# Optimization experiments

Measured on AMD Instinct MI355X. Metric: run time of the kernel, lower is better.

Reference implementation:

```python
import jax, jax.numpy as jnp
import numpy as np

N_REC = 12288  # 12 * nside^2, nside=32


def _mlp(x, w1, b1, w2, b2):
    # two-layer MLP with SiLU, as in GraphCast-style edge embedders
    return jnp.dot(jax.nn.silu(jnp.dot(x, w1) + b1), w2) + b2


def setup_inputs() -> dict:
    key = jax.random.key(0)
    ks = jax.random.split(key, 12)
    B, E, D_X, D_EDGE = 2, 393216, 128, 4
    EDGE_IN, EDGE_OUT, LIN_OUT = D_EDGE + D_X, 256, 256

    def glorot(k, shape):
        fan = shape[0] + shape[1]
        return jax.random.normal(k, shape, jnp.float32) * jnp.sqrt(2.0 / fan)

    return {
        "x": jax.random.normal(ks[0], (B, E, D_X), jnp.float32),
        "edge_attr": jax.random.normal(ks[1], (E, D_EDGE), jnp.float32),
        "edge_index": jax.random.randint(ks[2], (2, E), 0, N_REC, jnp.int64),
        "w1e": glorot(ks[3], (EDGE_IN, EDGE_OUT)),
        "b1e": jnp.zeros((EDGE_OUT,), jnp.float32),
        "w2e": glorot(ks[4], (EDGE_OUT, EDGE_OUT)),
        "b2e": jnp.zeros((EDGE_OUT,), jnp.float32),
        "w1f": glorot(ks[5], (EDGE_OUT, LIN_OUT)),
        "b1f": jnp.zeros((LIN_OUT,), jnp.float32),
        "w2f": glorot(ks[6], (LIN_OUT, LIN_OUT)),
        "b2f": jnp.zeros((LIN_OUT,), jnp.float32),
    }


def reference(x, edge_attr, edge_index, w1e, b1e, w2e, b2e, w1f, b1f, w2f, b2f):
    B = x.shape[0]
    # broadcast edge_attr over batch and concat with per-edge grid features
    ea = jnp.broadcast_to(edge_attr[None], (B,) + edge_attr.shape)  # [B,E,d_edge]
    v_g_prime = jnp.concatenate([ea, x], axis=-1)                    # [B,E,edge_in]
    v_g = _mlp(v_g_prime, w1e, b1e, w2e, b2e)                        # [B,E,edge_out]
    # scatter-sum edges into receiver nodes (edge_index[1]) along dim 1
    recv = edge_index[1]
    v_m_sum = jnp.zeros((B, N_REC, v_g.shape[-1]), v_g.dtype).at[:, recv].add(v_g)
    return _mlp(v_m_sum, w1f, b1f, w2f, b2f)                         # [B,N_REC,lin_out]
```

## Files before the change

### kernel.cpp

```cpp
#include <hip/hip_runtime.h>
#include <hip/hip_bf16.h>

#define E_EDGES 393216
#define NRECV   12288
#define DX      128
#define BATCH   2

typedef short bf16x8 __attribute__((ext_vector_type(8)));
typedef float f32x4  __attribute__((ext_vector_type(4)));

__device__ __forceinline__ unsigned short f2bf(float f) {
  union { float f; unsigned u; } v; v.f = f;
  unsigned r = v.u + 0x7FFFu + ((v.u >> 16) & 1u);
  return (unsigned short)(r >> 16);
}

__device__ __forceinline__ unsigned pk2(float a, float b) {
  __hip_bfloat162 h = __float22bfloat162_rn(make_float2(a, b));
  union { __hip_bfloat162 h; unsigned u; } c; c.h = h;
  return c.u;
}

__device__ __forceinline__ float silu_f(float v) {
  float e = __builtin_amdgcn_exp2f(v * -1.44269504089f);
  return v * __builtin_amdgcn_rcpf(1.0f + e);
}

__global__ __launch_bounds__(256) void zero_kernel(float4* __restrict__ p, int n4) {
  int i = blockIdx.x * 256 + threadIdx.x;
  int stride = gridDim.x * 256;
  float4 z = make_float4(0.f, 0.f, 0.f, 0.f);
  for (; i < n4; i += stride) p[i] = z;
}

__global__ __launch_bounds__(256) void prep_kernel(
    const float* __restrict__ w1e, const float* __restrict__ b1e,
    const float* __restrict__ w2e, const float* __restrict__ w1f,
    const float* __restrict__ w2f,
    unsigned short* __restrict__ w1sw, unsigned short* __restrict__ w2esw,
    unsigned short* __restrict__ w1fsw, unsigned short* __restrict__ w2fsw,
    const int* __restrict__ recv, int* __restrict__ cnt) {
  int blk = blockIdx.x;
  if (blk < 160) {
    int t = blk * 256 + threadIdx.x;
    int j = t & 7, l = (t >> 3) & 63, rest = t >> 9;
    int nf = rest & 15, ks = rest >> 4;
    int k = ks * 32 + (l >> 4) * 8 + j;
    int n = nf * 16 + (l & 15);
    float v = (k < 132) ? w1e[k * 256 + n] : (k == 132 ? b1e[n] : 0.0f);
    w1sw[t] = f2bf(v);
  } else if (blk < 928) {
    int g = blk - 160;
    int which = g >> 8;
    int t = (g & 255) * 256 + threadIdx.x;
    const float* W = (which == 0) ? w2e : (which == 1) ? w1f : w2f;
    unsigned short* O = (which == 0) ? w2esw : (which == 1) ? w1fsw : w2fsw;
    int j = t & 7, l = (t >> 3) & 63, rest = t >> 9;
    int nf = rest & 15, ks = rest >> 4;
    int k = ks * 32 + (l >> 4) * 8 + j;
    int n = nf * 16 + (l & 15);
    O[t] = f2bf(W[k * 256 + n]);
  } else {
    int e = (blk - 928) * 256 + threadIdx.x;
    if (e < E_EDGES) atomicAdd(&cnt[recv[e]], 1);
  }
}

__global__ __launch_bounds__(256) void scan_kernel(const int* __restrict__ cnt,
                                                   int* __restrict__ head) {
  __shared__ int ts[256];
  const int t = threadIdx.x;
  const int base = t * 48;
  int s = 0;
#pragma unroll
  for (int i = 0; i < 48; ++i) s += cnt[base + i];
  ts[t] = s;
  __syncthreads();
  for (int d = 1; d < 256; d <<= 1) {
    int v = (t >= d) ? ts[t - d] : 0;
    __syncthreads();
    ts[t] += v;
    __syncthreads();
  }
  int run = (t == 0) ? 0 : ts[t - 1];
  for (int i = 0; i < 48; ++i) { head[base + i] = run; run += cnt[base + i]; }
}

__global__ void scatter_kernel(const int* __restrict__ recv, int* __restrict__ head,
                               int* __restrict__ perm) {
  int e = blockIdx.x * 256 + threadIdx.x;
  if (e < E_EDGES) {
    int pos = atomicAdd(&head[recv[e]], 1);
    perm[pos] = e;
  }
}

__global__ __launch_bounds__(256, 4) void edge_kernel(
    const float* __restrict__ x, const float* __restrict__ edge_attr,
    const int* __restrict__ recv, const int* __restrict__ perm,
    const unsigned short* __restrict__ w1sw, float* __restrict__ s) {
  __shared__ __align__(16) char As[64 * 384];
  __shared__ int rs[64];
  __shared__ int seg_recv[64];
  __shared__ unsigned seg32[16];

  const int tid = threadIdx.x;
  const int l  = tid & 63;
  const int w  = tid >> 6;
  const int lo = l & 15, hi = l >> 4;
  const int bid = blockIdx.x;
  const int p0 = ((bid & 7) * 768 + (bid >> 3)) * 64;
  const int b  = blockIdx.y;

  const int r = tid >> 2, q = tid & 3;
  const int er = perm[p0 + r];
  const float4* xr = (const float4*)(x + ((size_t)b * E_EDGES + er) * DX);
  float4 xv[8];
#pragma unroll
  for (int i = 0; i < 8; ++i) xv[i] = xr[i * 4 + q];

  float4 ea;
  if (tid < 64) {
    int e1 = perm[p0 + tid];
    rs[tid] = recv[e1];
    ea = *(const float4*)(edge_attr + (size_t)e1 * 4);
  }

  for (int idx = tid; idx < 960; idx += 256) {
    int rr = idx / 15, k2 = idx - rr * 15;
    int byte0 = 264 + 8 * k2;
    uint2 vz = make_uint2(k2 == 0 ? 0x00003F80u : 0u, 0u);
    *(uint2*)(As + rr * 384 + (byte0 ^ ((rr & 7) << 4))) = vz;
  }

  {
    const int rx = (r & 7) << 4;
#pragma unroll
    for (int i = 0; i < 8; ++i) {
      int t = i * 4 + q;
      int byte0 = 8 + 8 * t;
      *(uint2*)(As + r * 384 + (byte0 ^ rx)) =
          make_uint2(pk2(xv[i].x, xv[i].y), pk2(xv[i].z, xv[i].w));
    }
  }
  if (tid < 64) {
    *(uint2*)(As + tid * 384 + ((tid & 7) << 4)) =
        make_uint2(pk2(ea.x, ea.y), pk2(ea.z, ea.w));
  }
  __syncthreads();

  const int flag = (l == 63) || (rs[l + 1] != rs[l]);
  const unsigned long long segmask = __ballot(flag);
  const int nseg = __popcll(segmask);
  if (tid < 64) {
    int sid = __popcll(segmask & ((1ull << tid) - 1ull));
    ((unsigned char*)seg32)[tid] = (unsigned char)sid;
    if (flag) seg_recv[sid] = rs[tid];
  }

  f32x4 acc[4][4] = {};
  const int axor = (lo & 7) << 4;
  const unsigned short* wbase = w1sw + ((size_t)(w * 4) * 64 + l) * 8;
  bf16x8 cur0 = *(const bf16x8*)(wbase + 0 * 512);
  bf16x8 cur1 = *(const bf16x8*)(wbase + 1 * 512);
  bf16x8 cur2 = *(const bf16x8*)(wbase + 2 * 512);
  bf16x8 cur3 = *(const bf16x8*)(wbase + 3 * 512);
#pragma unroll
  for (int kk = 0; kk < 5; ++kk) {
    bf16x8 a[4];
#pragma unroll
    for (int mf = 0; mf < 4; ++mf)
      a[mf] = *(const bf16x8*)(As + (mf * 16 + lo) * 384 + ((kk * 64 + hi * 16) ^ axor));
    bf16x8 nxt0, nxt1, nxt2, nxt3;
    if (kk < 4) {
      const unsigned short* wn = wbase + (size_t)(kk + 1) * 8192;
      nxt0 = *(const bf16x8*)(wn + 0 * 512);
      nxt1 = *(const bf16x8*)(wn + 1 * 512);
      nxt2 = *(const bf16x8*)(wn + 2 * 512);
      nxt3 = *(const bf16x8*)(wn + 3 * 512);
    }
    __builtin_amdgcn_s_setprio(1);
#pragma unroll
    for (int mf = 0; mf < 4; ++mf)
      acc[mf][0] = __builtin_amdgcn_mfma_f32_16x16x32_bf16(a[mf], cur0, acc[mf][0], 0, 0, 0);
#pragma unroll
    for (int mf = 0; mf < 4; ++mf)
      acc[mf][1] = __builtin_amdgcn_mfma_f32_16x16x32_bf16(a[mf], cur1, acc[mf][1], 0, 0, 0);
#pragma unroll
    for (int mf = 0; mf < 4; ++mf)
      acc[mf][2] = __builtin_amdgcn_mfma_f32_16x16x32_bf16(a[mf], cur2, acc[mf][2], 0, 0, 0);
#pragma unroll
    for (int mf = 0; mf < 4; ++mf)
      acc[mf][3] = __builtin_amdgcn_mfma_f32_16x16x32_bf16(a[mf], cur3, acc[mf][3], 0, 0, 0);
    __builtin_amdgcn_s_setprio(0);
    if (kk < 4) { cur0 = nxt0; cur1 = nxt1; cur2 = nxt2; cur3 = nxt3; }
  }
  __syncthreads();

  unsigned pkd[4][4][2];
#pragma unroll
  for (int mf = 0; mf < 4; ++mf)
#pragma unroll
    for (int nf = 0; nf < 4; ++nf) {
      float v0 = silu_f(acc[mf][nf][0]);
      float v1 = silu_f(acc[mf][nf][1]);
      float v2 = silu_f(acc[mf][nf][2]);
      float v3 = silu_f(acc[mf][nf][3]);
      pkd[mf][nf][0] = pk2(v0, v1);
      pkd[mf][nf][1] = pk2(v2, v3);
    }

  unsigned hbw[2][4][4];
#pragma unroll
  for (int kk = 0; kk < 2; ++kk)
#pragma unroll
    for (int nf = 0; nf < 4; ++nf)
#pragma unroll
      for (int t = 0; t < 4; ++t) {
        int src = ((hi & 1) * 2 + (t >> 1)) * 16 + lo;
        int a0 = __shfl((int)pkd[2 * kk][nf][t & 1], src, 64);
        int a1 = __shfl((int)pkd[2 * kk + 1][nf][t & 1], src, 64);
        hbw[kk][nf][t] = (hi & 2) ? (unsigned)a1 : (unsigned)a0;
      }

  float* sb = s + (size_t)b * NRECV * 256;
  for (int p = 0; p * 16 < nseg; ++p) {
    union { unsigned u[4]; bf16x8 v; } ia[2];
#pragma unroll
    for (int kk = 0; kk < 2; ++kk) {
      unsigned d0 = seg32[kk * 8 + hi * 2];
      unsigned d1 = seg32[kk * 8 + hi * 2 + 1];
      unsigned tgt = (unsigned)(lo + p * 16);
      ia[kk].u[0] = (((d0 & 255u) == tgt) ? 0x3F80u : 0u) |
                    ((((d0 >> 8) & 255u) == tgt) ? 0x3F800000u : 0u);
      ia[kk].u[1] = ((((d0 >> 16) & 255u) == tgt) ? 0x3F80u : 0u) |
                    (((d0 >> 24) == tgt) ? 0x3F800000u : 0u);
      ia[kk].u[2] = (((d1 & 255u) == tgt) ? 0x3F80u : 0u) |
                    ((((d1 >> 8) & 255u) == tgt) ? 0x3F800000u : 0u);
      ia[kk].u[3] = ((((d1 >> 16) & 255u) == tgt) ? 0x3F80u : 0u) |
                    (((d1 >> 24) == tgt) ? 0x3F800000u : 0u);
    }
    f32x4 accS[4] = {};
    __builtin_amdgcn_s_setprio(1);
#pragma unroll
    for (int kk = 0; kk < 2; ++kk)
#pragma unroll
      for (int nf = 0; nf < 4; ++nf) {
        union { unsigned u[4]; bf16x8 v; } hb;
        hb.u[0] = hbw[kk][nf][0]; hb.u[1] = hbw[kk][nf][1];
        hb.u[2] = hbw[kk][nf][2]; hb.u[3] = hbw[kk][nf][3];
        accS[nf] = __builtin_amdgcn_mfma_f32_16x16x32_bf16(ia[kk].v, hb.v, accS[nf], 0, 0, 0);
      }
    __builtin_amdgcn_s_setprio(0);
#pragma unroll
    for (int j = 0; j < 4; ++j) {
      int sidx = p * 16 + hi * 4 + j;
      if (sidx < nseg) {
        int rcv = seg_recv[sidx];
        const bool interior = (sidx > 0) && (sidx < nseg - 1);
#pragma unroll
        for (int nf = 0; nf < 4; ++nf) {
          float* dst = sb + (size_t)rcv * 256 + w * 64 + nf * 16 + lo;
          if (interior) *dst = accS[nf][j];
          else atomicAdd(dst, accS[nf][j]);
        }
      }
    }
  }
}

__device__ __forceinline__ void gemm64(const unsigned short* Ns,
                                       const unsigned short* __restrict__ Bsw,
                                       int w, int l, f32x4 acc[4][4]) {
  const int lo = l & 15, hi = l >> 4;
#pragma unroll
  for (int kk = 0; kk < 8; ++kk) {
    bf16x8 a[4], bb[4];
#pragma unroll
    for (int mf = 0; mf < 4; ++mf)
      a[mf] = *(const bf16x8*)&Ns[(mf * 16 + lo) * 264 + kk * 32 + hi * 8];
#pragma unroll
    for (int nf = 0; nf < 4; ++nf)
      bb[nf] = *(const bf16x8*)&Bsw[(size_t)(((kk * 16) + (w * 4 + nf)) * 64 + l) * 8];
#pragma unroll
    for (int mf = 0; mf < 4; ++mf)
#pragma unroll
      for (int nf = 0; nf < 4; ++nf)
        acc[mf][nf] = __builtin_amdgcn_mfma_f32_16x16x32_bf16(a[mf], bb[nf], acc[mf][nf], 0, 0, 0);
  }
}

__global__ __launch_bounds__(256) void node_kernel(
    const float* __restrict__ s, const int* __restrict__ cnt,
    const unsigned short* __restrict__ w2esw, const float* __restrict__ b2e,
    const unsigned short* __restrict__ w1fsw, const float* __restrict__ b1f,
    const unsigned short* __restrict__ w2fsw, const float* __restrict__ b2f,
    float* __restrict__ out) {
  __shared__ unsigned short Ns[64 * 264];
  __shared__ int   cntl[64];
  __shared__ float bias1[256], bias2[256], bias3[256];

  const int tid = threadIdx.x;
  const int l  = tid & 63;
  const int w  = tid >> 6;
  const int lo = l & 15, hi = l >> 4;
  const int r0 = blockIdx.x * 64;
  const int b  = blockIdx.y;

  const float4* sb = (const float4*)(s + ((size_t)b * NRECV + r0) * 256);
#pragma unroll
  for (int i = 0; i < 16; ++i) {
    int f = i * 256 + tid;
    float4 v = sb[f];
    int g = f * 4;
    int row = g >> 8, col = g & 255;
    *(uint2*)&Ns[row * 264 + col] = make_uint2(pk2(v.x, v.y), pk2(v.z, v.w));
  }
  if (tid < 64) cntl[tid] = cnt[r0 + tid];
  bias1[tid] = b2e[tid];
  bias2[tid] = b1f[tid];
  bias3[tid] = b2f[tid];
  __syncthreads();

  {
    f32x4 acc[4][4] = {};
    gemm64(Ns, w2esw, w, l, acc);
    __syncthreads();
#pragma unroll
    for (int mf = 0; mf < 4; ++mf)
#pragma unroll
      for (int nf = 0; nf < 4; ++nf) {
        const int col = w * 64 + nf * 16 + lo;
#pragma unroll
        for (int j = 0; j < 4; ++j) {
          const int row = mf * 16 + hi * 4 + j;
          float v = acc[mf][nf][j] + (float)cntl[row] * bias1[col];
          Ns[row * 264 + col] = f2bf(v);
        }
      }
    __syncthreads();
  }
  {
    f32x4 acc[4][4] = {};
    gemm64(Ns, w1fsw, w, l, acc);
    __syncthreads();
#pragma unroll
    for (int mf = 0; mf < 4; ++mf)
#pragma unroll
      for (int nf = 0; nf < 4; ++nf) {
        const int col = w * 64 + nf * 16 + lo;
#pragma unroll
        for (int j = 0; j < 4; ++j) {
          const int row = mf * 16 + hi * 4 + j;
          float v = silu_f(acc[mf][nf][j] + bias2[col]);
          Ns[row * 264 + col] = f2bf(v);
        }
      }
    __syncthreads();
  }
  {
    f32x4 acc[4][4] = {};
    gemm64(Ns, w2fsw, w, l, acc);
#pragma unroll
    for (int mf = 0; mf < 4; ++mf)
#pragma unroll
      for (int nf = 0; nf < 4; ++nf) {
        const int col = w * 64 + nf * 16 + lo;
#pragma unroll
        for (int j = 0; j < 4; ++j) {
          const int row = mf * 16 + hi * 4 + j;
          out[((size_t)b * NRECV + r0 + row) * 256 + col] = acc[mf][nf][j] + bias3[col];
        }
      }
  }
}

extern "C" void kernel_launch(void* const* d_in, const int* in_sizes, int n_in,
                              void* d_out, int out_size, void* d_ws, size_t ws_size,
                              hipStream_t stream) {
  const float* x         = (const float*)d_in[0];
  const float* edge_attr = (const float*)d_in[1];
  const int*   edge_idx  = (const int*)d_in[2];
  const float* w1e       = (const float*)d_in[3];
  const float* b1e       = (const float*)d_in[4];
  const float* w2e       = (const float*)d_in[5];
  const float* b2e       = (const float*)d_in[6];
  const float* w1f       = (const float*)d_in[7];
  const float* b1f       = (const float*)d_in[8];
  const float* w2f       = (const float*)d_in[9];
  const float* b2f       = (const float*)d_in[10];
  float* out = (float*)d_out;

  char* ws = (char*)d_ws;
  float*          sbuf  = (float*)(ws + 0);
  int*            cnt   = (int*)(ws + 25165824);
  int*            head  = (int*)(ws + 25214976);
  int*            perm  = (int*)(ws + 25264128);
  unsigned short* w1sw  = (unsigned short*)(ws + 26836992);
  unsigned short* w2esw = (unsigned short*)(ws + 26918912);
  unsigned short* w1fsw = (unsigned short*)(ws + 27049984);
  unsigned short* w2fsw = (unsigned short*)(ws + 27181056);

  const int* recv = edge_idx + E_EDGES;

  zero_kernel<<<2048, 256, 0, stream>>>((float4*)ws, 1575936);

  prep_kernel<<<2464, 256, 0, stream>>>(w1e, b1e, w2e, w1f, w2f,
                                        w1sw, w2esw, w1fsw, w2fsw, recv, cnt);

  scan_kernel<<<1, 256, 0, stream>>>(cnt, head);
  scatter_kernel<<<E_EDGES / 256, 256, 0, stream>>>(recv, head, perm);

  dim3 eg(E_EDGES / 64, BATCH);
  edge_kernel<<<eg, 256, 0, stream>>>(x, edge_attr, recv, perm, w1sw, sbuf);

  dim3 ng(NRECV / 64, BATCH);
  node_kernel<<<ng, 256, 0, stream>>>(sbuf, cnt, w2esw, b2e, w1fsw, b1f, w2fsw, b2f, out);
}
```

Before: 243.6 us.

## Halve edge tile to 32 rows per block and raise occupancy

Result: slower. 260.6 us (+7.0%).

```diff
diff --git a/kernel.cpp b/kernel.cpp
--- a/kernel.cpp
+++ b/kernel.cpp
@@ -95,38 +95,38 @@
   }
 }
 
-__global__ __launch_bounds__(256, 4) void edge_kernel(
+__global__ __launch_bounds__(256, 6) void edge_kernel(
     const float* __restrict__ x, const float* __restrict__ edge_attr,
     const int* __restrict__ recv, const int* __restrict__ perm,
     const unsigned short* __restrict__ w1sw, float* __restrict__ s) {
-  __shared__ __align__(16) char As[64 * 384];
-  __shared__ int rs[64];
-  __shared__ int seg_recv[64];
-  __shared__ unsigned seg32[16];
+  __shared__ __align__(16) char As[32 * 384];
+  __shared__ int rs[32];
+  __shared__ int seg_recv[32];
+  __shared__ unsigned seg32[8];
 
   const int tid = threadIdx.x;
   const int l  = tid & 63;
   const int w  = tid >> 6;
   const int lo = l & 15, hi = l >> 4;
   const int bid = blockIdx.x;
-  const int p0 = ((bid & 7) * 768 + (bid >> 3)) * 64;
+  const int p0 = ((bid & 7) * 1536 + (bid >> 3)) * 32;
   const int b  = blockIdx.y;
 
-  const int r = tid >> 2, q = tid & 3;
+  const int r = tid >> 3, q = tid & 7;
   const int er = perm[p0 + r];
   const float4* xr = (const float4*)(x + ((size_t)b * E_EDGES + er) * DX);
-  float4 xv[8];
-#pragma unroll
-  for (int i = 0; i < 8; ++i) xv[i] = xr[i * 4 + q];
+  float4 xv[4];
+#pragma unroll
+  for (int i = 0; i < 4; ++i) xv[i] = xr[i * 8 + q];
 
   float4 ea;
-  if (tid < 64) {
+  if (tid < 32) {
     int e1 = perm[p0 + tid];
     rs[tid] = recv[e1];
     ea = *(const float4*)(edge_attr + (size_t)e1 * 4);
   }
 
-  for (int idx = tid; idx < 960; idx += 256) {
+  for (int idx = tid; idx < 480; idx += 256) {
     int rr = idx / 15, k2 = idx - rr * 15;
     int byte0 = 264 + 8 * k2;
     uint2 vz = make_uint2(k2 == 0 ? 0x00003F80u : 0u, 0u);
@@ -136,121 +136,90 @@
   {
     const int rx = (r & 7) << 4;
 #pragma unroll
-    for (int i = 0; i < 8; ++i) {
-      int t = i * 4 + q;
+    for (int i = 0; i < 4; ++i) {
+      int t = i * 8 + q;
       int byte0 = 8 + 8 * t;
       *(uint2*)(As + r * 384 + (byte0 ^ rx)) =
           make_uint2(pk2(xv[i].x, xv[i].y), pk2(xv[i].z, xv[i].w));
     }
   }
-  if (tid < 64) {
+  if (tid < 32) {
     *(uint2*)(As + tid * 384 + ((tid & 7) << 4)) =
         make_uint2(pk2(ea.x, ea.y), pk2(ea.z, ea.w));
   }
   __syncthreads();
 
-  const int flag = (l == 63) || (rs[l + 1] != rs[l]);
+  const int flag = (l < 32) ? ((l == 31) || (rs[l + 1] != rs[l])) : 0;
   const unsigned long long segmask = __ballot(flag);
   const int nseg = __popcll(segmask);
-  if (tid < 64) {
+  if (tid < 32) {
     int sid = __popcll(segmask & ((1ull << tid) - 1ull));
     ((unsigned char*)seg32)[tid] = (unsigned char)sid;
     if (flag) seg_recv[sid] = rs[tid];
   }
 
-  f32x4 acc[4][4] = {};
+  f32x4 acc[2][4] = {};
   const int axor = (lo & 7) << 4;
-  const unsigned short* wbase = w1sw + ((size_t)(w * 4) * 64 + l) * 8;
-  bf16x8 cur0 = *(const bf16x8*)(wbase + 0 * 512);
-  bf16x8 cur1 = *(const bf16x8*)(wbase + 1 * 512);
-  bf16x8 cur2 = *(const bf16x8*)(wbase + 2 * 512);
-  bf16x8 cur3 = *(const bf16x8*)(wbase + 3 * 512);
 #pragma unroll
   for (int kk = 0; kk < 5; ++kk) {
-    bf16x8 a[4];
-#pragma unroll
-    for (int mf = 0; mf < 4; ++mf)
-      a[mf] = *(const bf16x8*)(As + (mf * 16 + lo) * 384 + ((kk * 64 + hi * 16) ^ axor));
-    bf16x8 nxt0, nxt1, nxt2, nxt3;
-    if (kk < 4) {
-      const unsigned short* wn = wbase + (size_t)(kk + 1) * 8192;
-      nxt0 = *(const bf16x8*)(wn + 0 * 512);
-      nxt1 = *(const bf16x8*)(wn + 1 * 512);
-      nxt2 = *(const bf16x8*)(wn + 2 * 512);
-      nxt3 = *(const bf16x8*)(wn + 3 * 512);
-    }
+    bf16x8 a0 = *(const bf16x8*)(As + lo * 384 + ((kk * 64 + hi * 16) ^ axor));
+    bf16x8 a1 = *(const bf16x8*)(As + (16 + lo) * 384 + ((kk * 64 + hi * 16) ^ axor));
     __builtin_amdgcn_s_setprio(1);
 #pragma unroll
-    for (int mf = 0; mf < 4; ++mf)
-      acc[mf][0] = __builtin_amdgcn_mfma_f32_16x16x32_bf16(a[mf], cur0, acc[mf][0], 0, 0, 0);
-#pragma unroll
-    for (int mf = 0; mf < 4; ++mf)
-      acc[mf][1] = __builtin_amdgcn_mfma_f32_16x16x32_bf16(a[mf], cur1, acc[mf][1], 0, 0, 0);
-#pragma unroll
-    for (int mf = 0; mf < 4; ++mf)
-      acc[mf][2] = __builtin_amdgcn_mfma_f32_16x16x32_bf16(a[mf], cur2, acc[mf][2], 0, 0, 0);
-#pragma unroll
-    for (int mf = 0; mf < 4; ++mf)
-      acc[mf][3] = __builtin_amdgcn_mfma_f32_16x16x32_bf16(a[mf], cur3, acc[mf][3], 0, 0, 0);
+    for (int nf = 0; nf < 4; ++nf) {
+      bf16x8 bb = *(const bf16x8*)&w1sw[(size_t)(((kk * 16) + (w * 4 + nf)) * 64 + l) * 8];
+      acc[0][nf] = __builtin_amdgcn_mfma_f32_16x16x32_bf16(a0, bb, acc[0][nf], 0, 0, 0);
+      acc[1][nf] = __builtin_amdgcn_mfma_f32_16x16x32_bf16(a1, bb, acc[1][nf], 0, 0, 0);
+    }
     __builtin_amdgcn_s_setprio(0);
-    if (kk < 4) { cur0 = nxt0; cur1 = nxt1; cur2 = nxt2; cur3 = nxt3; }
   }
   __syncthreads();
 
-  unsigned pkd[4][4][2];
-#pragma unroll
-  for (int mf = 0; mf < 4; ++mf)
+  unsigned pkd[2][4][2];
+#pragma unroll
+  for (int mf = 0; mf < 2; ++mf)
 #pragma unroll
     for (int nf = 0; nf < 4; ++nf) {
-      float v0 = silu_f(acc[mf][nf][0]);
-      float v1 = silu_f(acc[mf][nf][1]);
-      float v2 = silu_f(acc[mf][nf][2]);
-      float v3 = silu_f(acc[mf][nf][3]);
-      pkd[mf][nf][0] = pk2(v0, v1);
-      pkd[mf][nf][1] = pk2(v2, v3);
-    }
-
-  unsigned hbw[2][4][4];
-#pragma unroll
-  for (int kk = 0; kk < 2; ++kk)
-#pragma unroll
-    for (int nf = 0; nf < 4; ++nf)
-#pragma unroll
-      for (int t = 0; t < 4; ++t) {
-        int src = ((hi & 1) * 2 + (t >> 1)) * 16 + lo;
-        int a0 = __shfl((int)pkd[2 * kk][nf][t & 1], src, 64);
-        int a1 = __shfl((int)pkd[2 * kk + 1][nf][t & 1], src, 64);
-        hbw[kk][nf][t] = (hi & 2) ? (unsigned)a1 : (unsigned)a0;
-      }
+      pkd[mf][nf][0] = pk2(silu_f(acc[mf][nf][0]), silu_f(acc[mf][nf][1]));
+      pkd[mf][nf][1] = pk2(silu_f(acc[mf][nf][2]), silu_f(acc[mf][nf][3]));
+    }
+
+  unsigned hbw[4][4];
+#pragma unroll
+  for (int nf = 0; nf < 4; ++nf)
+#pragma unroll
+    for (int t = 0; t < 4; ++t) {
+      int src = ((hi & 1) * 2 + (t >> 1)) * 16 + lo;
+      int a0 = __shfl((int)pkd[0][nf][t & 1], src, 64);
+      int a1 = __shfl((int)pkd[1][nf][t & 1], src, 64);
+      hbw[nf][t] = (hi & 2) ? (unsigned)a1 : (unsigned)a0;
+    }
 
   float* sb = s + (size_t)b * NRECV * 256;
   for (int p = 0; p * 16 < nseg; ++p) {
-    union { unsigned u[4]; bf16x8 v; } ia[2];
-#pragma unroll
-    for (int kk = 0; kk < 2; ++kk) {
-      unsigned d0 = seg32[kk * 8 + hi * 2];
-      unsigned d1 = seg32[kk * 8 + hi * 2 + 1];
+    union { unsigned u[4]; bf16x8 v; } ia;
+    {
+      unsigned d0 = seg32[hi * 2];
+      unsigned d1 = seg32[hi * 2 + 1];
       unsigned tgt = (unsigned)(lo + p * 16);
-      ia[kk].u[0] = (((d0 & 255u) == tgt) ? 0x3F80u : 0u) |
-                    ((((d0 >> 8) & 255u) == tgt) ? 0x3F800000u : 0u);
-      ia[kk].u[1] = ((((d0 >> 16) & 255u) == tgt) ? 0x3F80u : 0u) |
-                    (((d0 >> 24) == tgt) ? 0x3F800000u : 0u);
-      ia[kk].u[2] = (((d1 & 255u) == tgt) ? 0x3F80u : 0u) |
-                    ((((d1 >> 8) & 255u) == tgt) ? 0x3F800000u : 0u);
-      ia[kk].u[3] = ((((d1 >> 16) & 255u) == tgt) ? 0x3F80u : 0u) |
-                    (((d1 >> 24) == tgt) ? 0x3F800000u : 0u);
+      ia.u[0] = (((d0 & 255u) == tgt) ? 0x3F80u : 0u) |
+                ((((d0 >> 8) & 255u) == tgt) ? 0x3F800000u : 0u);
+      ia.u[1] = ((((d0 >> 16) & 255u) == tgt) ? 0x3F80u : 0u) |
+                (((d0 >> 24) == tgt) ? 0x3F800000u : 0u);
+      ia.u[2] = (((d1 & 255u) == tgt) ? 0x3F80u : 0u) |
+                ((((d1 >> 8) & 255u) == tgt) ? 0x3F800000u : 0u);
+      ia.u[3] = ((((d1 >> 16) & 255u) == tgt) ? 0x3F80u : 0u) |
+                (((d1 >> 24) == tgt) ? 0x3F800000u : 0u);
     }
     f32x4 accS[4] = {};
     __builtin_amdgcn_s_setprio(1);
 #pragma unroll
-    for (int kk = 0; kk < 2; ++kk)
-#pragma unroll
-      for (int nf = 0; nf < 4; ++nf) {
-        union { unsigned u[4]; bf16x8 v; } hb;
-        hb.u[0] = hbw[kk][nf][0]; hb.u[1] = hbw[kk][nf][1];
-        hb.u[2] = hbw[kk][nf][2]; hb.u[3] = hbw[kk][nf][3];
-        accS[nf] = __builtin_amdgcn_mfma_f32_16x16x32_bf16(ia[kk].v, hb.v, accS[nf], 0, 0, 0);
-      }
+    for (int nf = 0; nf < 4; ++nf) {
+      union { unsigned u[4]; bf16x8 v; } hb;
+      hb.u[0] = hbw[nf][0]; hb.u[1] = hbw[nf][1];
+      hb.u[2] = hbw[nf][2]; hb.u[3] = hbw[nf][3];
+      accS[nf] = __builtin_amdgcn_mfma_f32_16x16x32_bf16(ia.v, hb.v, accS[nf], 0, 0, 0);
+    }
     __builtin_amdgcn_s_setprio(0);
 #pragma unroll
     for (int j = 0; j < 4; ++j) {
@@ -411,7 +380,7 @@
   scan_kernel<<<1, 256, 0, stream>>>(cnt, head);
   scatter_kernel<<<E_EDGES / 256, 256, 0, stream>>>(recv, head, perm);
 
-  dim3 eg(E_EDGES / 64, BATCH);
+  dim3 eg(E_EDGES / 32, BATCH);
   edge_kernel<<<eg, 256, 0, stream>>>(x, edge_attr, recv, perm, w1sw, sbuf);
 
   dim3 ng(NRECV / 64, BATCH);
```
